# Performance work log

Measured on AMD Instinct MI355X. Metric: run time of the kernel, lower is better.

## Reference

```python
import jax, jax.numpy as jnp
import numpy as np

NUM_HEADS = 8
DIMS = 512
SR = 2
EPS = 1e-6


def setup_inputs() -> dict:
    key = jax.random.key(0)
    ks = jax.random.split(key, 12)
    B, H, W, C = 4, 64, 64, DIMS
    s = 0.02
    return {
        "x": jax.random.normal(ks[0], (B, H * W, C), dtype=jnp.float32),
        "Wq": jax.random.normal(ks[1], (C, DIMS), dtype=jnp.float32) * s,
        "bq": jnp.zeros((DIMS,), jnp.float32),
        "Wk": jax.random.normal(ks[2], (C, DIMS), dtype=jnp.float32) * s,
        "bk": jnp.zeros((DIMS,), jnp.float32),
        "Wv": jax.random.normal(ks[3], (C, DIMS), dtype=jnp.float32) * s,
        "bv": jnp.zeros((DIMS,), jnp.float32),
        "Wp": jax.random.normal(ks[4], (DIMS, DIMS), dtype=jnp.float32) * s,
        "bp": jnp.zeros((DIMS,), jnp.float32),
        "sr_w": jax.random.normal(ks[5], (SR, SR, C, DIMS), dtype=jnp.float32) * s,  # HWIO
        "sr_b": jnp.zeros((DIMS,), jnp.float32),
        "ln_g": jnp.ones((DIMS,), jnp.float32),
        "ln_b": jnp.zeros((DIMS,), jnp.float32),
        "H": 64,
        "W": 64,
    }


def reference(x, Wq, bq, Wk, bk, Wv, bv, Wp, bp, sr_w, sr_b, ln_g, ln_b, H, W):
    B, N, C = x.shape
    hd = DIMS // NUM_HEADS

    # spatial-reduction of K/V: strided conv (kernel=stride=SR, SAME) + LayerNorm
    kv = x.reshape(B, H, W, C)
    kv = jax.lax.conv_general_dilated(
        kv, sr_w, window_strides=(SR, SR), padding="SAME",
        dimension_numbers=("NHWC", "HWIO", "NHWC")) + sr_b
    kv = kv.reshape(B, -1, C)  # [B, Nk, C], Nk = (H//SR)*(W//SR)
    mu = jnp.mean(kv, axis=-1, keepdims=True)
    var = jnp.mean(jnp.square(kv - mu), axis=-1, keepdims=True)
    kv = (kv - mu) * jax.lax.rsqrt(var + EPS) * ln_g + ln_b
    Nk = kv.shape[1]

    # NOTE: original splits heads as reshape(B, N, head_dims, num_heads) and
    # indexes the LAST axis per head -> head h sees channels d*NUM_HEADS+h.
    q = (x @ Wq + bq).reshape(B, N, hd, NUM_HEADS)
    k = (kv @ Wk + bk).reshape(B, Nk, hd, NUM_HEADS)
    v = (kv @ Wv + bv).reshape(B, Nk, hd, NUM_HEADS)

    scores = jnp.einsum("bqdh,bkdh->bhqk", q, k) / jnp.sqrt(jnp.float32(hd))
    w = jax.nn.softmax(scores, axis=-1)
    # concat of heads along channels -> (B, N, NUM_HEADS, hd) layout
    out = jnp.einsum("bhqk,bkdh->bqhd", w, v).reshape(B, N, DIMS)
    return out @ Wp + bp
```

## Files before the change

### kernel.cpp

```cpp
#include <hip/hip_runtime.h>


typedef __attribute__((ext_vector_type(8))) _Float16 f16x8;
typedef __attribute__((ext_vector_type(4))) _Float16 f16x4;
typedef __attribute__((ext_vector_type(4))) float f32x4;

#define EXP2F(x) __builtin_amdgcn_exp2f(x)

__device__ __forceinline__ void gload_lds16(const _Float16* g, _Float16* l)
{
    __builtin_amdgcn_global_load_lds(
        (const __attribute__((address_space(1))) void*)g,
        (__attribute__((address_space(3))) void*)l, 16, 0, 0);
}

template<int N>
__device__ __forceinline__ void wait_vm()
{
    asm volatile("s_waitcnt vmcnt(%0)" :: "n"(N) : "memory");
}

__global__ __launch_bounds__(256)
void prep_k(const float* __restrict__ x,
            const float* __restrict__ Wq, const float* __restrict__ Wk,
            const float* __restrict__ Wv, const float* __restrict__ Wp,
            const float* __restrict__ srw,
            _Float16* __restrict__ xh, _Float16* __restrict__ wqt,
            _Float16* __restrict__ wkvt, _Float16* __restrict__ wpt,
            _Float16* __restrict__ srwt)
{
    __shared__ float T[32][33];
    const int id = blockIdx.x;
    const int t = threadIdx.x;

    if (id < 4096) {
        const size_t i = ((size_t)id * 256 + t) * 8;
        const float4 a = *(const float4*)(x + i);
        const float4 b = *(const float4*)(x + i + 4);
        f16x8 o;
        o[0] = (_Float16)a.x; o[1] = (_Float16)a.y; o[2] = (_Float16)a.z; o[3] = (_Float16)a.w;
        o[4] = (_Float16)b.x; o[5] = (_Float16)b.y; o[6] = (_Float16)b.z; o[7] = (_Float16)b.w;
        *(f16x8*)(xh + i) = o;
        return;
    }

    if (id < 5120) {
        const int id2 = id - 4096;
        const int z = id2 >> 8, k0 = ((id2 >> 4) & 15) * 32, n0 = (id2 & 15) * 32;
        const float* src; _Float16* dst; int perm;
        switch (z) {
            case 0:  src = Wq; dst = wqt;           perm = 1; break;
            case 1:  src = Wk; dst = wkvt;          perm = 1; break;
            case 2:  src = Wv; dst = wkvt + 262144; perm = 0; break;
            default: src = Wp; dst = wpt;           perm = 0; break;
        }
        {
            const int r = t >> 3, c = (t & 7) * 4;
            const float4 v = *(const float4*)(src + (size_t)(k0 + r) * 512 + n0 + c);
            T[r][c + 0] = v.x; T[r][c + 1] = v.y; T[r][c + 2] = v.z; T[r][c + 3] = v.w;
        }
        __syncthreads();
        {
            const int j = t >> 3, i0 = (t & 7) * 4;
            const int n = n0 + j;
            const int nper = perm ? ((n & 7) * 64 + (n >> 3)) : n;
            f16x4 o;
            o[0] = (_Float16)T[i0 + 0][j];
            o[1] = (_Float16)T[i0 + 1][j];
            o[2] = (_Float16)T[i0 + 2][j];
            o[3] = (_Float16)T[i0 + 3][j];
            *(f16x4*)(dst + (size_t)nper * 512 + k0 + i0) = o;
        }
        return;
    }

    {
        const int id3 = id - 5120;
        const int n0 = (id3 & 15) * 32, k0 = (id3 >> 4) * 32;
        {
            const int r = t >> 3, c = (t & 7) * 4;
            const float4 v = *(const float4*)(srw + (size_t)(k0 + r) * 512 + n0 + c);
            T[r][c + 0] = v.x; T[r][c + 1] = v.y; T[r][c + 2] = v.z; T[r][c + 3] = v.w;
        }
        __syncthreads();
        {
            const int j = t >> 3, i0 = (t & 7) * 4;
            f16x4 o;
            o[0] = (_Float16)T[i0 + 0][j];
            o[1] = (_Float16)T[i0 + 1][j];
            o[2] = (_Float16)T[i0 + 2][j];
            o[3] = (_Float16)T[i0 + 3][j];
            *(f16x4*)(srwt + (size_t)(n0 + j) * 2048 + k0 + i0) = o;
        }
        return;
    }
}

template<int MODE, bool CONV, int BM>
__device__ __forceinline__ void gemm_body(
    const int bx, const int by,
    const _Float16* __restrict__ A, const _Float16* __restrict__ Wt,
    const float* __restrict__ bias, const float* __restrict__ bias2,
    void* __restrict__ Cv, void* __restrict__ Cv2,
    _Float16* __restrict__ As, _Float16* __restrict__ Ws)
{
    constexpr int K = CONV ? 2048 : 512;
    constexpr int NIT = K / 32;
    constexpr int MT = BM / 32;
    constexpr int AI = BM / 64;
    constexpr int ABUF = BM * 32;
    constexpr int NBUF = (BM == 64) ? 4 : 3;
    constexpr int P = NBUF - 1;
    constexpr int L = AI + 2;
    const int tid = threadIdx.x;
    const int wave = tid >> 6, lane = tid & 63;
    const int quad = lane >> 4, l15 = lane & 15;
    const int wm = wave >> 1, wn = wave & 1;
    const int wrow = wm * (BM / 2);
    const int m0 = by * BM, n0 = bx * 128;

    const _Float16* abase[AI];
    int ac8[AI];
    #pragma unroll
    for (int t = 0; t < AI; ++t) {
        const int e = (wave * AI + t) * 64 + lane;
        const int row = e >> 2, c8 = (e & 3) * 8;
        ac8[t] = c8;
        if (CONV) {
            const int grow = m0 + row;
            const int b = grow >> 10, rem = grow & 1023;
            const int oh = rem >> 5, ow = rem & 31;
            abase[t] = A + ((size_t)((b * 64 + 2 * oh) * 64) + 2 * ow) * 512;
        } else {
            abase[t] = A + (size_t)(m0 + row) * K + c8;
        }
    }
    const _Float16* wbase[2];
    #pragma unroll
    for (int t = 0; t < 2; ++t) {
        const int e = (wave * 2 + t) * 64 + lane;
        const int row = e >> 2, c8 = (e & 3) * 8;
        wbase[t] = Wt + (size_t)(n0 + row) * K + c8;
    }

    auto stage = [&](const int k0, const int buf) {
        #pragma unroll
        for (int t = 0; t < AI; ++t) {
            const _Float16* gp;
            if (CONV) {
                const int gk = k0 + ac8[t];
                gp = abase[t] + ((gk >> 10) & 1) * 32768 + ((gk >> 9) & 1) * 512
                              + (gk & 511);
            } else {
                gp = abase[t] + k0;
            }
            gload_lds16(gp, &As[buf * ABUF + (wave * AI + t) * 512]);
        }
        #pragma unroll
        for (int t = 0; t < 2; ++t)
            gload_lds16(wbase[t] + k0, &Ws[buf * 4096 + (wave * 2 + t) * 512]);
    };

    f32x4 acc[MT][4] = {};

    #pragma unroll
    for (int p = 0; p < P; ++p) stage(p * 32, p);

    int cur = 0, nxt = P % NBUF;
    for (int it = 0; it < NIT; ++it) {
        int rem = NIT - 1 - it;
        if (rem > P - 1) rem = P - 1;
        switch (rem) {
            case 0:  wait_vm<0>(); break;
            case 1:  wait_vm<L>(); break;
            case 2:  wait_vm<2 * L>(); break;
            default: wait_vm<3 * L>(); break;
        }
        __builtin_amdgcn_s_barrier();
        __builtin_amdgcn_sched_barrier(0);
        if (it + P < NIT) {
            stage((it + P) * 32, nxt);
            nxt = (nxt + 1 == NBUF) ? 0 : nxt + 1;
        }

        f16x8 af[MT], bf[4];
        #pragma unroll
        for (int mt = 0; mt < MT; ++mt)
            af[mt] = *(const f16x8*)&As[cur * ABUF + (wrow + mt * 16 + l15) * 32 + quad * 8];
        #pragma unroll
        for (int nt = 0; nt < 4; ++nt)
            bf[nt] = *(const f16x8*)&Ws[cur * 4096 + (wn * 64 + nt * 16 + l15) * 32 + quad * 8];
        #pragma unroll
        for (int mt = 0; mt < MT; ++mt)
            #pragma unroll
            for (int nt = 0; nt < 4; ++nt)
                acc[mt][nt] = __builtin_amdgcn_mfma_f32_16x16x32_f16(
                    af[mt], bf[nt], acc[mt][nt], 0, 0, 0);

        cur = (cur + 1 == NBUF) ? 0 : cur + 1;
    }

    #pragma unroll
    for (int nt = 0; nt < 4; ++nt) {
        const int gcol = n0 + wn * 64 + nt * 16 + l15;
        float bv;
        if (MODE == 6) bv = bias[(gcol & 63) * 8 + (gcol >> 6)];
        else if (MODE == 5) bv = (gcol < 512) ? bias[(gcol & 63) * 8 + (gcol >> 6)]
                                              : bias2[gcol - 512];
        else bv = bias[gcol];
        #pragma unroll
        for (int mt = 0; mt < MT; ++mt) {
            const int row0 = m0 + wrow + mt * 16 + quad * 4;
            if (MODE == 0) {
                #pragma unroll
                for (int r = 0; r < 4; ++r)
                    ((float*)Cv)[(size_t)(row0 + r) * 512 + gcol] = acc[mt][nt][r] + bv;
            } else if (MODE == 4 || MODE == 6) {
                #pragma unroll
                for (int r = 0; r < 4; ++r)
                    ((_Float16*)Cv)[(size_t)(row0 + r) * 512 + gcol] =
                        (_Float16)(acc[mt][nt][r] + bv);
            } else {
                if (gcol < 512) {
                    #pragma unroll
                    for (int r = 0; r < 4; ++r)
                        ((_Float16*)Cv)[(size_t)(row0 + r) * 512 + gcol] =
                            (_Float16)(acc[mt][nt][r] + bv);
                } else {
                    const int c = gcol - 512;
                    const int h = c & 7, d = c >> 3;
                    const int b_ = row0 >> 10, jj = row0 & 1023;
                    f16x4 o;
                    #pragma unroll
                    for (int r = 0; r < 4; ++r) o[r] = (_Float16)(acc[mt][nt][r] + bv);
                    *(f16x4*)((_Float16*)Cv2 +
                              ((size_t)(b_ * 8 + h) * 64 + d) * 1024 + jj) = o;
                }
            }
        }
    }
}

template<int MODE, bool CONV, int BM>
__global__ __launch_bounds__(256)
void gemm_f16(const _Float16* __restrict__ A, const _Float16* __restrict__ Wt,
              const float* __restrict__ bias, const float* __restrict__ bias2,
              void* __restrict__ Cv, void* __restrict__ Cv2)
{
    __shared__ __align__(16) _Float16 lds[24576];
    constexpr int NBUF = (BM == 64) ? 4 : 3;
    gemm_body<MODE, CONV, BM>(blockIdx.x, blockIdx.y, A, Wt, bias, bias2,
                              Cv, Cv2, lds, lds + NBUF * BM * 32);
}

__global__ __launch_bounds__(256)
void convq_k(const _Float16* __restrict__ xh, const _Float16* __restrict__ srwt,
             const float* __restrict__ srb, const _Float16* __restrict__ wqt,
             const float* __restrict__ bq,
             _Float16* __restrict__ kvh, _Float16* __restrict__ qh)
{
    __shared__ __align__(16) _Float16 lds[24576];
    const int id = blockIdx.x;
    if (id < 256) {
        gemm_body<4, true, 64>(id & 3, id >> 2, xh, srwt, srb, nullptr,
                               kvh, nullptr, lds, lds + 4 * 64 * 32);
    } else {
        const int id2 = id - 256;
        gemm_body<6, false, 128>(id2 & 3, id2 >> 2, xh, wqt, bq, nullptr,
                                 qh, nullptr, lds, lds + 3 * 128 * 32);
    }
}

__global__ __launch_bounds__(256)
void ln_k(_Float16* __restrict__ buf, const float* __restrict__ g,
          const float* __restrict__ b)
{
    const int row = blockIdx.x;
    _Float16* p = buf + (size_t)row * 512;
    const int tid = threadIdx.x;
    const float vx = (float)p[tid * 2], vy = (float)p[tid * 2 + 1];
    float s = vx + vy, q = vx * vx + vy * vy;
    #pragma unroll
    for (int off = 32; off > 0; off >>= 1) {
        s += __shfl_xor(s, off);
        q += __shfl_xor(q, off);
    }
    __shared__ float ss[4], sq[4], stat[2];
    const int wid = tid >> 6;
    if ((tid & 63) == 0) { ss[wid] = s; sq[wid] = q; }
    __syncthreads();
    if (tid == 0) {
        const float S = ss[0] + ss[1] + ss[2] + ss[3];
        const float Q = sq[0] + sq[1] + sq[2] + sq[3];
        const float mu = S * (1.f / 512.f);
        const float var = fmaxf(Q * (1.f / 512.f) - mu * mu, 0.f);
        stat[0] = mu;
        stat[1] = rsqrtf(var + 1e-6f);
    }
    __syncthreads();
    const float mu = stat[0], rs = stat[1];
    const float2 gg = *(const float2*)(g + tid * 2);
    const float2 bb = *(const float2*)(b + tid * 2);
    p[tid * 2]     = (_Float16)((vx - mu) * rs * gg.x + bb.x);
    p[tid * 2 + 1] = (_Float16)((vy - mu) * rs * gg.y + bb.y);
}

__global__ __launch_bounds__(512, 4)
void attn_mfma_k(const _Float16* __restrict__ qb,
                 const _Float16* __restrict__ kbuf,
                 const _Float16* __restrict__ vbuf,
                 _Float16* __restrict__ out)
{
    const int bh = blockIdx.y;
    const int qt = blockIdx.x;
    const int b = bh >> 3, h = bh & 7;
    const int tid = threadIdx.x;
    const int wave = tid >> 6, lane = tid & 63;
    const int quad = lane >> 4, l15 = lane & 15;

    __shared__ __align__(16) _Float16 Ks[2][64 * 72];
    __shared__ __align__(16) _Float16 Vs[2][64 * 72];

    const int qrow = b * 4096 + qt * 256 + wave * 32 + l15;
    const _Float16* qp = qb + (size_t)qrow * 512 + h * 64 + quad * 8;
    f16x8 qf[2][2];
    #pragma unroll
    for (int su = 0; su < 2; ++su) {
        qf[su][0] = *(const f16x8*)(qp + su * 16 * 512);
        qf[su][1] = *(const f16x8*)(qp + su * 16 * 512 + 32);
    }
    {
        const _Float16 qs = (_Float16)0.18033688f;
        #pragma unroll
        for (int su = 0; su < 2; ++su)
            #pragma unroll
            for (int g = 0; g < 2; ++g)
                #pragma unroll
                for (int i = 0; i < 8; ++i) qf[su][g][i] *= qs;
    }

    f16x8 ones;
    #pragma unroll
    for (int i = 0; i < 8; ++i) ones[i] = (_Float16)1.0f;

    const int kr = tid >> 3, kc = (tid & 7) * 8;
    const int krp = (kr & 32) | ((kr & 4) << 2) | ((kr >> 1) & 12) | (kr & 3);
    const _Float16* kg = kbuf + (size_t)(b * 1024 + kr) * 512 + h * 64 + kc;
    const _Float16* vg = vbuf + (size_t)(bh * 64 + kr) * 1024 + kc;

    f16x8 krg = *(const f16x8*)kg;
    f16x8 vrg = *(const f16x8*)vg;
    *(f16x8*)&Ks[0][krp * 72 + kc] = krg;
    *(f16x8*)&Vs[0][kr * 72 + kc] = vrg;

    f32x4 acc[2][4] = {};
    f32x4 acc_l[2] = {};

    for (int kt = 0; kt < 16; ++kt) {
        const int cur = kt & 1;
        __syncthreads();
        if (kt < 15) {
            krg = *(const f16x8*)(kg + (size_t)(kt + 1) * 64 * 512);
            vrg = *(const f16x8*)(vg + (kt + 1) * 64);
        }

        #pragma unroll
        for (int kb = 0; kb < 2; ++kb) {
            f16x8 pa[2];
            #pragma unroll
            for (int c = 0; c < 2; ++c) {
                const int ct = kb * 2 + c;
                const f16x8 kf0 = *(const f16x8*)&Ks[cur][(ct * 16 + l15) * 72 + quad * 8];
                const f16x8 kf1 = *(const f16x8*)&Ks[cur][(ct * 16 + l15) * 72 + 32 + quad * 8];
                #pragma unroll
                for (int su = 0; su < 2; ++su) {
                    f32x4 s = {};
                    s = __builtin_amdgcn_mfma_f32_16x16x32_f16(kf0, qf[su][0], s, 0, 0, 0);
                    s = __builtin_amdgcn_mfma_f32_16x16x32_f16(kf1, qf[su][1], s, 0, 0, 0);
                    pa[su][c * 4 + 0] = (_Float16)EXP2F(s[0]);
                    pa[su][c * 4 + 1] = (_Float16)EXP2F(s[1]);
                    pa[su][c * 4 + 2] = (_Float16)EXP2F(s[2]);
                    pa[su][c * 4 + 3] = (_Float16)EXP2F(s[3]);
                }
            }
            __builtin_amdgcn_s_setprio(1);
            #pragma unroll
            for (int su = 0; su < 2; ++su)
                acc_l[su] = __builtin_amdgcn_mfma_f32_16x16x32_f16(
                    pa[su], ones, acc_l[su], 0, 0, 0);
            #pragma unroll
            for (int nt = 0; nt < 4; ++nt) {
                const f16x8 vf = *(const f16x8*)&Vs[cur][(nt * 16 + l15) * 72 + kb * 32 + quad * 8];
                #pragma unroll
                for (int su = 0; su < 2; ++su)
                    acc[su][nt] = __builtin_amdgcn_mfma_f32_16x16x32_f16(
                        pa[su], vf, acc[su][nt], 0, 0, 0);
            }
            __builtin_amdgcn_s_setprio(0);
        }

        if (kt < 15) {
            *(f16x8*)&Ks[cur ^ 1][krp * 72 + kc] = krg;
            *(f16x8*)&Vs[cur ^ 1][kr * 72 + kc] = vrg;
        }
    }

    #pragma unroll
    for (int su = 0; su < 2; ++su) {
        float inv[4];
        #pragma unroll
        for (int r = 0; r < 4; ++r) inv[r] = 1.0f / acc_l[su][r];
        #pragma unroll
        for (int nt = 0; nt < 4; ++nt)
            #pragma unroll
            for (int r = 0; r < 4; ++r) {
                const int row = qt * 256 + wave * 32 + su * 16 + quad * 4 + r;
                const int col = h * 64 + nt * 16 + l15;
                out[((size_t)b * 4096 + row) * 512 + col] =
                    (_Float16)(acc[su][nt][r] * inv[r]);
            }
    }
}

extern "C" void kernel_launch(void* const* d_in, const int* in_sizes, int n_in,
                              void* d_out, int out_size, void* d_ws, size_t ws_size,
                              hipStream_t stream)
{
    const float* x   = (const float*)d_in[0];
    const float* Wq  = (const float*)d_in[1];
    const float* bq  = (const float*)d_in[2];
    const float* Wk  = (const float*)d_in[3];
    const float* bk  = (const float*)d_in[4];
    const float* Wv  = (const float*)d_in[5];
    const float* bv  = (const float*)d_in[6];
    const float* Wp  = (const float*)d_in[7];
    const float* bp  = (const float*)d_in[8];
    const float* srw = (const float*)d_in[9];
    const float* srb = (const float*)d_in[10];
    const float* lng = (const float*)d_in[11];
    const float* lnb = (const float*)d_in[12];

    _Float16* ws   = (_Float16*)d_ws;
    _Float16* xh   = ws;
    _Float16* atth = xh + 8388608;
    _Float16* kvh  = atth + 8388608;
    _Float16* kh   = kvh + 2097152;
    _Float16* vh   = kh + 2097152;
    _Float16* wqt  = vh + 2097152;
    _Float16* wkvt = wqt + 262144;
    _Float16* wpt  = wkvt + 524288;
    _Float16* srwt = wpt + 262144;
    _Float16* qh   = (_Float16*)d_out;

    prep_k<<<6144, 256, 0, stream>>>(x, Wq, Wk, Wv, Wp, srw,
                                     xh, wqt, wkvt, wpt, srwt);
    convq_k<<<768, 256, 0, stream>>>(xh, srwt, srb, wqt, bq, kvh, qh);
    ln_k<<<4096, 256, 0, stream>>>(kvh, lng, lnb);
    gemm_f16<5, false, 64><<<dim3(8, 64), 256, 0, stream>>>(
        kvh, wkvt, bk, bv, kh, vh);
    attn_mfma_k<<<dim3(16, 32), 512, 0, stream>>>(qh, kh, vh, atth);
    gemm_f16<0, false, 128><<<dim3(4, 128), 256, 0, stream>>>(
        atth, wpt, bp, nullptr, d_out, nullptr);
}
```

Measured before the change: 215.6 us.

## Fuse LayerNorm into KV projection GEMM and double attention rows per wave

After: 210.0 us. -2.6%, faster.

```diff
diff --git a/kernel.cpp b/kernel.cpp
--- a/kernel.cpp
+++ b/kernel.cpp
@@ -205,8 +205,6 @@
         const int gcol = n0 + wn * 64 + nt * 16 + l15;
         float bv;
         if (MODE == 6) bv = bias[(gcol & 63) * 8 + (gcol >> 6)];
-        else if (MODE == 5) bv = (gcol < 512) ? bias[(gcol & 63) * 8 + (gcol >> 6)]
-                                              : bias2[gcol - 512];
         else bv = bias[gcol];
         #pragma unroll
         for (int mt = 0; mt < MT; ++mt) {
@@ -215,27 +213,11 @@
                 #pragma unroll
                 for (int r = 0; r < 4; ++r)
                     ((float*)Cv)[(size_t)(row0 + r) * 512 + gcol] = acc[mt][nt][r] + bv;
-            } else if (MODE == 4 || MODE == 6) {
+            } else {
                 #pragma unroll
                 for (int r = 0; r < 4; ++r)
                     ((_Float16*)Cv)[(size_t)(row0 + r) * 512 + gcol] =
                         (_Float16)(acc[mt][nt][r] + bv);
-            } else {
-                if (gcol < 512) {
-                    #pragma unroll
-                    for (int r = 0; r < 4; ++r)
-                        ((_Float16*)Cv)[(size_t)(row0 + r) * 512 + gcol] =
-                            (_Float16)(acc[mt][nt][r] + bv);
-                } else {
-                    const int c = gcol - 512;
-                    const int h = c & 7, d = c >> 3;
-                    const int b_ = row0 >> 10, jj = row0 & 1023;
-                    f16x4 o;
-                    #pragma unroll
-                    for (int r = 0; r < 4; ++r) o[r] = (_Float16)(acc[mt][nt][r] + bv);
-                    *(f16x4*)((_Float16*)Cv2 +
-                              ((size_t)(b_ * 8 + h) * 64 + d) * 1024 + jj) = o;
-                }
             }
         }
     }
@@ -272,40 +254,139 @@
 }
 
 __global__ __launch_bounds__(256)
-void ln_k(_Float16* __restrict__ buf, const float* __restrict__ g,
-          const float* __restrict__ b)
-{
-    const int row = blockIdx.x;
-    _Float16* p = buf + (size_t)row * 512;
+void kvln_k(const _Float16* __restrict__ A, const _Float16* __restrict__ Wt,
+            const float* __restrict__ lng, const float* __restrict__ lnb,
+            const float* __restrict__ biask, const float* __restrict__ biasv,
+            _Float16* __restrict__ kh, _Float16* __restrict__ vh)
+{
+    __shared__ __align__(16) _Float16 Al[64 * 512];
+    __shared__ __align__(16) _Float16 Ws[2 * 4096];
+    const int bx = blockIdx.x, by = blockIdx.y;
     const int tid = threadIdx.x;
-    const float vx = (float)p[tid * 2], vy = (float)p[tid * 2 + 1];
-    float s = vx + vy, q = vx * vx + vy * vy;
-    #pragma unroll
-    for (int off = 32; off > 0; off >>= 1) {
-        s += __shfl_xor(s, off);
-        q += __shfl_xor(q, off);
-    }
-    __shared__ float ss[4], sq[4], stat[2];
-    const int wid = tid >> 6;
-    if ((tid & 63) == 0) { ss[wid] = s; sq[wid] = q; }
+    const int wave = tid >> 6, lane = tid & 63;
+    const int quad = lane >> 4, l15 = lane & 15;
+    const int wm = wave >> 1, wn = wave & 1;
+    const int wrow = wm * 32;
+    const int m0 = by * 64, n0 = bx * 128;
+
+    const _Float16* wbase[2];
+    #pragma unroll
+    for (int t = 0; t < 2; ++t) {
+        const int e = (wave * 2 + t) * 64 + lane;
+        const int row = e >> 2, c8 = (e & 3) * 8;
+        wbase[t] = Wt + (size_t)(n0 + row) * 512 + c8;
+    }
+    auto stageW = [&](const int k0, const int buf) {
+        #pragma unroll
+        for (int t = 0; t < 2; ++t)
+            gload_lds16(wbase[t] + k0, &Ws[buf * 4096 + (wave * 2 + t) * 512]);
+    };
+    stageW(0, 0);
+
+    const int colt = (tid & 63) * 8;
+    float g[8], bb[8];
+    {
+        const float4 g0 = *(const float4*)(lng + colt);
+        const float4 g1 = *(const float4*)(lng + colt + 4);
+        const float4 b0 = *(const float4*)(lnb + colt);
+        const float4 b1 = *(const float4*)(lnb + colt + 4);
+        g[0] = g0.x; g[1] = g0.y; g[2] = g0.z; g[3] = g0.w;
+        g[4] = g1.x; g[5] = g1.y; g[6] = g1.z; g[7] = g1.w;
+        bb[0] = b0.x; bb[1] = b0.y; bb[2] = b0.z; bb[3] = b0.w;
+        bb[4] = b1.x; bb[5] = b1.y; bb[6] = b1.z; bb[7] = b1.w;
+    }
+    const _Float16* ab = A + (size_t)m0 * 512;
+    #pragma unroll
+    for (int r4 = 0; r4 < 4; ++r4) {
+        float f[4][8]; float mu[4], rs[4];
+        #pragma unroll
+        for (int i = 0; i < 4; ++i) {
+            const int c = (r4 * 4 + i) * 256 + tid;
+            const f16x8 d = *(const f16x8*)(ab + (size_t)c * 8);
+            #pragma unroll
+            for (int e = 0; e < 8; ++e) f[i][e] = (float)d[e];
+        }
+        #pragma unroll
+        for (int i = 0; i < 4; ++i) {
+            float s = 0.f, q = 0.f;
+            #pragma unroll
+            for (int e = 0; e < 8; ++e) { s += f[i][e]; q += f[i][e] * f[i][e]; }
+            #pragma unroll
+            for (int off = 32; off > 0; off >>= 1) {
+                s += __shfl_xor(s, off);
+                q += __shfl_xor(q, off);
+            }
+            mu[i] = s * (1.f / 512.f);
+            rs[i] = rsqrtf(fmaxf(q * (1.f / 512.f) - mu[i] * mu[i], 0.f) + 1e-6f);
+        }
+        #pragma unroll
+        for (int i = 0; i < 4; ++i) {
+            const int row = (r4 * 4 + i) * 4 + wave;
+            f16x8 o;
+            #pragma unroll
+            for (int e = 0; e < 8; ++e)
+                o[e] = (_Float16)((f[i][e] - mu[i]) * rs[i] * g[e] + bb[e]);
+            const int boff = (row * 1024 + colt * 2) ^ ((row & 7) << 4);
+            *(f16x8*)((char*)Al + boff) = o;
+        }
+    }
     __syncthreads();
-    if (tid == 0) {
-        const float S = ss[0] + ss[1] + ss[2] + ss[3];
-        const float Q = sq[0] + sq[1] + sq[2] + sq[3];
-        const float mu = S * (1.f / 512.f);
-        const float var = fmaxf(Q * (1.f / 512.f) - mu * mu, 0.f);
-        stat[0] = mu;
-        stat[1] = rsqrtf(var + 1e-6f);
-    }
-    __syncthreads();
-    const float mu = stat[0], rs = stat[1];
-    const float2 gg = *(const float2*)(g + tid * 2);
-    const float2 bb = *(const float2*)(b + tid * 2);
-    p[tid * 2]     = (_Float16)((vx - mu) * rs * gg.x + bb.x);
-    p[tid * 2 + 1] = (_Float16)((vy - mu) * rs * gg.y + bb.y);
-}
-
-__global__ __launch_bounds__(512, 4)
+
+    f32x4 acc[2][4] = {};
+    int cur = 0;
+    for (int it = 0; it < 16; ++it) {
+        if (it) {
+            wait_vm<0>();
+            __builtin_amdgcn_s_barrier();
+        }
+        if (it + 1 < 16) stageW((it + 1) * 32, cur ^ 1);
+        const int k0 = it * 32;
+        f16x8 af[2], bf[4];
+        #pragma unroll
+        for (int mt = 0; mt < 2; ++mt) {
+            const int row = wrow + mt * 16 + l15;
+            const int boff = (row * 1024 + k0 * 2 + quad * 16) ^ ((row & 7) << 4);
+            af[mt] = *(const f16x8*)((const char*)Al + boff);
+        }
+        #pragma unroll
+        for (int nt = 0; nt < 4; ++nt)
+            bf[nt] = *(const f16x8*)&Ws[cur * 4096 + (wn * 64 + nt * 16 + l15) * 32 + quad * 8];
+        #pragma unroll
+        for (int mt = 0; mt < 2; ++mt)
+            #pragma unroll
+            for (int nt = 0; nt < 4; ++nt)
+                acc[mt][nt] = __builtin_amdgcn_mfma_f32_16x16x32_f16(
+                    af[mt], bf[nt], acc[mt][nt], 0, 0, 0);
+        cur ^= 1;
+    }
+
+    #pragma unroll
+    for (int nt = 0; nt < 4; ++nt) {
+        const int gcol = n0 + wn * 64 + nt * 16 + l15;
+        const float bv = (gcol < 512) ? biask[(gcol & 63) * 8 + (gcol >> 6)]
+                                      : biasv[gcol - 512];
+        #pragma unroll
+        for (int mt = 0; mt < 2; ++mt) {
+            const int row0 = m0 + wrow + mt * 16 + quad * 4;
+            if (gcol < 512) {
+                #pragma unroll
+                for (int r = 0; r < 4; ++r)
+                    kh[(size_t)(row0 + r) * 512 + gcol] =
+                        (_Float16)(acc[mt][nt][r] + bv);
+            } else {
+                const int c = gcol - 512;
+                const int h = c & 7, d = c >> 3;
+                const int b_ = row0 >> 10, jj = row0 & 1023;
+                f16x4 o;
+                #pragma unroll
+                for (int r = 0; r < 4; ++r) o[r] = (_Float16)(acc[mt][nt][r] + bv);
+                *(f16x4*)(vh + ((size_t)(b_ * 8 + h) * 64 + d) * 1024 + jj) = o;
+            }
+        }
+    }
+}
+
+__global__ __launch_bounds__(512)
 void attn_mfma_k(const _Float16* __restrict__ qb,
                  const _Float16* __restrict__ kbuf,
                  const _Float16* __restrict__ vbuf,
@@ -321,18 +402,18 @@
     __shared__ __align__(16) _Float16 Ks[2][64 * 72];
     __shared__ __align__(16) _Float16 Vs[2][64 * 72];
 
-    const int qrow = b * 4096 + qt * 256 + wave * 32 + l15;
+    const int qrow = b * 4096 + qt * 512 + wave * 64 + l15;
     const _Float16* qp = qb + (size_t)qrow * 512 + h * 64 + quad * 8;
-    f16x8 qf[2][2];
-    #pragma unroll
-    for (int su = 0; su < 2; ++su) {
+    f16x8 qf[4][2];
+    #pragma unroll
+    for (int su = 0; su < 4; ++su) {
         qf[su][0] = *(const f16x8*)(qp + su * 16 * 512);
         qf[su][1] = *(const f16x8*)(qp + su * 16 * 512 + 32);
     }
     {
         const _Float16 qs = (_Float16)0.18033688f;
         #pragma unroll
-        for (int su = 0; su < 2; ++su)
+        for (int su = 0; su < 4; ++su)
             #pragma unroll
             for (int g = 0; g < 2; ++g)
                 #pragma unroll
@@ -353,8 +434,8 @@
     *(f16x8*)&Ks[0][krp * 72 + kc] = krg;
     *(f16x8*)&Vs[0][kr * 72 + kc] = vrg;
 
-    f32x4 acc[2][4] = {};
-    f32x4 acc_l[2] = {};
+    f32x4 acc[4][4] = {};
+    f32x4 acc_l[4] = {};
 
     for (int kt = 0; kt < 16; ++kt) {
         const int cur = kt & 1;
@@ -366,14 +447,14 @@
 
         #pragma unroll
         for (int kb = 0; kb < 2; ++kb) {
-            f16x8 pa[2];
+            f16x8 pa[4];
             #pragma unroll
             for (int c = 0; c < 2; ++c) {
                 const int ct = kb * 2 + c;
                 const f16x8 kf0 = *(const f16x8*)&Ks[cur][(ct * 16 + l15) * 72 + quad * 8];
                 const f16x8 kf1 = *(const f16x8*)&Ks[cur][(ct * 16 + l15) * 72 + 32 + quad * 8];
                 #pragma unroll
-                for (int su = 0; su < 2; ++su) {
+                for (int su = 0; su < 4; ++su) {
                     f32x4 s = {};
                     s = __builtin_amdgcn_mfma_f32_16x16x32_f16(kf0, qf[su][0], s, 0, 0, 0);
                     s = __builtin_amdgcn_mfma_f32_16x16x32_f16(kf1, qf[su][1], s, 0, 0, 0);
@@ -385,14 +466,14 @@
             }
             __builtin_amdgcn_s_setprio(1);
             #pragma unroll
-            for (int su = 0; su < 2; ++su)
+            for (int su = 0; su < 4; ++su)
                 acc_l[su] = __builtin_amdgcn_mfma_f32_16x16x32_f16(
                     pa[su], ones, acc_l[su], 0, 0, 0);
             #pragma unroll
             for (int nt = 0; nt < 4; ++nt) {
                 const f16x8 vf = *(const f16x8*)&Vs[cur][(nt * 16 + l15) * 72 + kb * 32 + quad * 8];
                 #pragma unroll
-                for (int su = 0; su < 2; ++su)
+                for (int su = 0; su < 4; ++su)
                     acc[su][nt] = __builtin_amdgcn_mfma_f32_16x16x32_f16(
                         pa[su], vf, acc[su][nt], 0, 0, 0);
             }
@@ -406,7 +487,7 @@
     }
 
     #pragma unroll
-    for (int su = 0; su < 2; ++su) {
+    for (int su = 0; su < 4; ++su) {
         float inv[4];
         #pragma unroll
         for (int r = 0; r < 4; ++r) inv[r] = 1.0f / acc_l[su][r];
@@ -414,7 +495,7 @@
         for (int nt = 0; nt < 4; ++nt)
             #pragma unroll
             for (int r = 0; r < 4; ++r) {
-                const int row = qt * 256 + wave * 32 + su * 16 + quad * 4 + r;
+                const int row = qt * 512 + wave * 64 + su * 16 + quad * 4 + r;
                 const int col = h * 64 + nt * 16 + l15;
                 out[((size_t)b * 4096 + row) * 512 + col] =
                     (_Float16)(acc[su][nt][r] * inv[r]);
@@ -455,10 +536,8 @@
     prep_k<<<6144, 256, 0, stream>>>(x, Wq, Wk, Wv, Wp, srw,
                                      xh, wqt, wkvt, wpt, srwt);
     convq_k<<<768, 256, 0, stream>>>(xh, srwt, srb, wqt, bq, kvh, qh);
-    ln_k<<<4096, 256, 0, stream>>>(kvh, lng, lnb);
-    gemm_f16<5, false, 64><<<dim3(8, 64), 256, 0, stream>>>(
-        kvh, wkvt, bk, bv, kh, vh);
-    attn_mfma_k<<<dim3(16, 32), 512, 0, stream>>>(qh, kh, vh, atth);
+    kvln_k<<<dim3(8, 64), 256, 0, stream>>>(kvh, wkvt, lng, lnb, bk, bv, kh, vh);
+    attn_mfma_k<<<dim3(8, 32), 512, 0, stream>>>(qh, kh, vh, atth);
     gemm_f16<0, false, 128><<<dim3(4, 128), 256, 0, stream>>>(
         atth, wpt, bp, nullptr, d_out, nullptr);
 }
```
